# Kernel optimization log

Hardware: AMD Instinct MI355X
Metric: run time of the kernel (lower is better)

Reference implementation:

```python
import jax, jax.numpy as jnp
import numpy as np

E = 256        # HP.EMBED_SIZE
R = 8          # number of derivation rules / MLPs
S = 512        # number of sequential derivation steps
N = 256        # nodes produced per step
N_INIT = 1024  # initial axiom (thax) embeddings
TOTAL = N_INIT + S * N  # 132096 rows in the vectors buffer
M = 65536      # masked nodes fed to eval_net


def setup_inputs() -> dict:
    key = jax.random.key(0)
    ks = jax.random.split(key, 12)
    rng = np.random.default_rng(0)

    init_vecs = jax.random.normal(ks[0], (N_INIT, E), jnp.float32)
    # rule MLPs: concat(2 parents) -> E (relu) -> E
    W1 = jax.random.normal(ks[1], (R, 2 * E, E), jnp.float32) * (1.0 / np.sqrt(2 * E))
    b1 = jnp.zeros((R, E), jnp.float32)
    W2 = jax.random.normal(ks[2], (R, E, E), jnp.float32) * (1.0 / np.sqrt(E))
    b2 = jnp.zeros((R, E), jnp.float32)
    # eval net: E -> E (relu) -> 1
    eval_W1 = jax.random.normal(ks[3], (E, E), jnp.float32) * (1.0 / np.sqrt(E))
    eval_b1 = jnp.zeros((E,), jnp.float32)
    eval_W2 = jax.random.normal(ks[4], (E, 1), jnp.float32) * (1.0 / np.sqrt(E))
    eval_b2 = jnp.zeros((1,), jnp.float32)

    # step s writes rows [N_INIT + s*N, N_INIT + (s+1)*N)
    ind_steps = (N_INIT + np.arange(S * N, dtype=np.int32)).reshape(S, N)
    # parents drawn causally from already-computed prefix [0, N_INIT + s*N)
    highs = (N_INIT + np.arange(S, dtype=np.int64) * N)[:, None, None]
    pars_ind_steps = (rng.random((S, N, 2)) * highs).astype(np.int32)
    rule_steps = rng.integers(0, R, size=(S,)).astype(np.int32)
    mask = rng.integers(0, TOTAL, size=(M,)).astype(np.int32)

    pos = jax.random.uniform(ks[5], (M,), jnp.float32)
    neg = jax.random.uniform(ks[6], (M,), jnp.float32)
    target = jnp.round(jax.random.uniform(ks[7], (M,), jnp.float32))

    return {
        'init_vecs': init_vecs, 'W1': W1, 'b1': b1, 'W2': W2, 'b2': b2,
        'eval_W1': eval_W1, 'eval_b1': eval_b1, 'eval_W2': eval_W2, 'eval_b2': eval_b2,
        'pos': pos, 'neg': neg, 'target': target,
        'ind_steps': jnp.asarray(ind_steps), 'pars_ind_steps': jnp.asarray(pars_ind_steps),
        'rule_steps': jnp.asarray(rule_steps), 'mask': jnp.asarray(mask),
    }


def reference(init_vecs, W1, b1, W2, b2, eval_W1, eval_b1, eval_W2, eval_b2,
              pos, neg, target, ind_steps, pars_ind_steps, rule_steps, mask):
    vectors = jnp.zeros((TOTAL, E), init_vecs.dtype).at[:N_INIT].set(init_vecs)

    def step(vec, xs):
        inds, pars, r = xs            # [N], [N,2], scalar rule id
        p = vec[pars].reshape(N, 2 * E)   # gather parents
        h = jax.nn.relu(p @ W1[r] + b1[r])
        out = h @ W2[r] + b2[r]
        return vec.at[inds].set(out), None  # scatter new node embeddings

    vectors, _ = jax.lax.scan(step, vectors, (ind_steps, pars_ind_steps, rule_steps))

    x = vectors[mask]
    val = (jax.nn.relu(x @ eval_W1 + eval_b1) @ eval_W2 + eval_b2)[:, 0]

    # pos_weight = POS_WEIGHT_EXTRA * tot_neg / tot_pos (constant w.r.t. grads)
    pw = jax.lax.stop_gradient(jnp.sum(neg) / jnp.maximum(jnp.sum(pos), 1.0))
    # BCEWithLogitsLoss(pos_weight, reduction='none')
    contrib = pw * target * jax.nn.softplus(-val) + (1.0 - target) * jax.nn.softplus(val)
    loss = jnp.sum((pos + neg) * contrib)
    posOK = jnp.sum(pos * (val >= 0))
    negOK = jnp.sum(neg * (val < 0))
    return loss, posOK, negOK
```

## Files before the change

### kernel.cpp

```cpp
#include <hip/hip_runtime.h>
#include <math.h>

#define EMB   256
#define TWOE  512
#define NINIT 1024
#define NSTEP 512
#define NPS   256
#define TOTAL (NINIT + NSTEP * NPS)
#define MM    65536
#define NNODE (NSTEP * NPS)
#define NKEY  2048
#define BTH   512
#define TROWS 32
#define CHK_SH  16384
#define RULE_SH (24 * CHK_SH)

typedef short s16x8 __attribute__((ext_vector_type(8)));
typedef float f32x4 __attribute__((ext_vector_type(4)));

#define OFF_VECH   0ull
#define OFF_VECL   ((size_t)TOTAL * EMB * 2)
#define OFF_VAL    (2ull * (size_t)TOTAL * EMB * 2)
#define OFF_CNT    (OFF_VAL + (size_t)MM * 4)
#define OFF_ACC    (OFF_CNT + 4096)
#define OFF_PW     (OFF_ACC + 64)
#define OFF_KCNT   (OFF_PW + 192)
#define OFF_KOFS   (OFF_KCNT + (size_t)NKEY * 4)
#define OFF_NL     (OFF_KOFS + (size_t)NKEY * 4)
#define OFF_BROWS  (OFF_NL + 256)
#define OFF_LVL8   (OFF_BROWS + (size_t)NNODE * 4)
#define OFF_WSPLIT (OFF_LVL8 + 132352)


__device__ __forceinline__ void store_dev_u32(unsigned* p, unsigned v) {
  asm volatile("global_store_dword %0, %1, off sc0 sc1" :: "v"(p), "v"(v) : "memory");
}
__device__ __forceinline__ void store_dev_b64(void* p, uint2 v) {
  asm volatile("global_store_dwordx2 %0, %1, off sc0 sc1" :: "v"(p), "v"(v) : "memory");
}
__device__ __forceinline__ void store_dev_b128(void* p, uint4 v) {
  store_dev_b64(p, make_uint2(v.x, v.y));
  store_dev_b64((char*)p + 8, make_uint2(v.z, v.w));
}
__device__ __forceinline__ unsigned load_dev_u32(const unsigned* p) {
  unsigned r;
  asm volatile("global_load_dword %0, %1, off sc0 sc1\n\ts_waitcnt vmcnt(0)"
               : "=v"(r) : "v"(p) : "memory");
  return r;
}

__device__ __forceinline__ void gbar_tree(unsigned* cnt, int xcd) {
  asm volatile("s_waitcnt vmcnt(0)" ::: "memory");
  __syncthreads();
  if (threadIdx.x == 0) {
    unsigned* xarr = cnt + 32 * xcd;
    unsigned* garr = cnt + 512;
    unsigned* gep  = cnt + 544;
    unsigned* xep  = cnt + 576 + 32 * xcd;
    unsigned o = __hip_atomic_fetch_add(xarr, 1u, __ATOMIC_RELAXED, __HIP_MEMORY_SCOPE_AGENT);
    unsigned tgt = o / 32u + 1u;
    if ((o & 31u) == 31u) {
      unsigned g = __hip_atomic_fetch_add(garr, 1u, __ATOMIC_RELAXED, __HIP_MEMORY_SCOPE_AGENT);
      unsigned gt = g / 8u + 1u;
      if ((g & 7u) == 7u) store_dev_u32(gep, gt);
      else while (load_dev_u32(gep) < gt) __builtin_amdgcn_s_sleep(1);
      store_dev_u32(xep, tgt);
    } else {
      while (load_dev_u32(xep) < tgt) __builtin_amdgcn_s_sleep(1);
    }
  }
  __syncthreads();
}

__device__ __forceinline__ void split8(const float* f, uint4& h4, uint4& l4) {
  unsigned hu[8], lu[8];
  #pragma unroll
  for (int i = 0; i < 8; ++i) {
    unsigned u = __builtin_bit_cast(unsigned, f[i]);
    float rh = __builtin_bit_cast(float, u & 0xffff0000u);
    float rl = f[i] - rh;
    hu[i] = u >> 16;
    lu[i] = __builtin_bit_cast(unsigned, rl) >> 16;
  }
  h4 = make_uint4(hu[0] | (hu[1] << 16), hu[2] | (hu[3] << 16),
                  hu[4] | (hu[5] << 16), hu[6] | (hu[7] << 16));
  l4 = make_uint4(lu[0] | (lu[1] << 16), lu[2] | (lu[3] << 16),
                  lu[4] | (lu[5] << 16), lu[6] | (lu[7] << 16));
}

__global__ void zero_scratch(unsigned* cnt, double* acc) {
  for (int i = threadIdx.x; i < 1024; i += 256) cnt[i] = 0u;
  if (threadIdx.x < 8) acc[threadIdx.x] = 0.0;
}

__global__ void init_convert(const float* __restrict__ src,
                             unsigned short* __restrict__ vh,
                             unsigned short* __restrict__ vl) {
  int slot = blockIdx.x * blockDim.x + threadIdx.x;
  float f[8];
  *(float4*)&f[0] = reinterpret_cast<const float4*>(src)[slot * 2];
  *(float4*)&f[4] = reinterpret_cast<const float4*>(src)[slot * 2 + 1];
  uint4 h4, l4;
  split8(f, h4, l4);
  *(uint4*)(vh + (size_t)slot * 8) = h4;
  *(uint4*)(vl + (size_t)slot * 8) = l4;
}

__global__ __launch_bounds__(512)
void presplit(const float* __restrict__ W1, const float* __restrict__ W2,
              short* __restrict__ Ws)
{
  const int blk = blockIdx.x;
  const int r = blk / 24, c = blk % 24;
  const float* src; int kbase;
  if (c < 16) { src = W1 + (size_t)r * TWOE * EMB; kbase = c * 32; }
  else        { src = W2 + (size_t)r * EMB * EMB;  kbase = (c - 16) * 32; }
  short* dst = Ws + (size_t)blk * CHK_SH;
  const int tid = threadIdx.x;
  #pragma unroll
  for (int u = 0; u < 2; ++u) {
    int qq = tid + u * 512;
    int g = qq >> 6, l = qq & 63;
    const float* p = src + (size_t)(kbase + ((l >> 4) << 3)) * EMB + (g << 4) + (l & 15);
    float f[8];
    #pragma unroll
    for (int i = 0; i < 8; ++i) f[i] = p[i * EMB];
    uint4 h4, l4;
    split8(f, h4, l4);
    *(uint4*)(dst + (size_t)qq * 8) = h4;
    *(uint4*)(dst + 8192 + (size_t)qq * 8) = l4;
  }
}

__global__ __launch_bounds__(256)
void prepass_levels(const int* __restrict__ pars, unsigned char* __restrict__ lvl8,
                    int* __restrict__ nlp)
{
  __shared__ unsigned char slvl[TOTAL];
  __shared__ int swmax[4];
  const int t = threadIdx.x;
  for (int i = t; i < NINIT; i += 256) slvl[i] = 0;
  __syncthreads();
  int Pa[8], Pb[8];
  #pragma unroll
  for (int w = 0; w < 8; ++w) {
    Pa[w] = pars[2 * (w * NPS + t)];
    Pb[w] = pars[2 * (w * NPS + t) + 1];
  }
  int lmax = 0;
  for (int s0 = 0; s0 < NSTEP; s0 += 8) {
    int Na[8], Nb[8];
    if (s0 + 8 < NSTEP) {
      #pragma unroll
      for (int w = 0; w < 8; ++w) {
        Na[w] = pars[2 * ((s0 + 8 + w) * NPS + t)];
        Nb[w] = pars[2 * ((s0 + 8 + w) * NPS + t) + 1];
      }
    } else {
      #pragma unroll
      for (int w = 0; w < 8; ++w) { Na[w] = 0; Nb[w] = 0; }
    }
    #pragma unroll
    for (int w = 0; w < 8; ++w) {
      int l1 = slvl[Pa[w]], l2 = slvl[Pb[w]];
      int lv = 1 + (l1 > l2 ? l1 : l2);
      slvl[NINIT + (s0 + w) * NPS + t] = (unsigned char)lv;
      if (lv > lmax) lmax = lv;
      __syncthreads();
    }
    #pragma unroll
    for (int w = 0; w < 8; ++w) { Pa[w] = Na[w]; Pb[w] = Nb[w]; }
  }
  const unsigned* sv = (const unsigned*)slvl;
  unsigned* gv = (unsigned*)lvl8;
  for (int i = t; i < TOTAL / 4; i += 256) gv[i] = sv[i];
  for (int o = 32; o; o >>= 1) lmax = max(lmax, __shfl_down(lmax, o));
  if ((t & 63) == 0) swmax[t >> 6] = lmax;
  __syncthreads();
  if (t == 0) {
    int m = 0;
    for (int w = 0; w < 4; ++w) m = max(m, swmax[w]);
    nlp[0] = m;
  }
}

__global__ __launch_bounds__(1024)
void prepass_bucket(const unsigned char* __restrict__ lvl8, const int* __restrict__ rules,
                    int* __restrict__ kcnt, int* __restrict__ kofs,
                    int* __restrict__ brows)
{
  __shared__ int scnt[NKEY];
  __shared__ int sofs[NKEY];
  const int t = threadIdx.x;
  for (int k = t; k < NKEY; k += 1024) scnt[k] = 0;
  __syncthreads();
  for (int i = t; i < NNODE; i += 1024) {
    int key = (int)lvl8[NINIT + i] * 8 + rules[i >> 8];
    atomicAdd(&scnt[key], 1);
  }
  __syncthreads();
  if (t == 0) {
    int run = 0;
    for (int k = 0; k < NKEY; ++k) {
      sofs[k] = run; kofs[k] = run; kcnt[k] = scnt[k]; run += scnt[k];
    }
  }
  __syncthreads();
  for (int i = t; i < NNODE; i += 1024) {
    int key = (int)lvl8[NINIT + i] * 8 + rules[i >> 8];
    int pos = atomicAdd(&sofs[key], 1);
    brows[pos] = i;
  }
}

__global__ __launch_bounds__(BTH, 1)
void scan_kernel(const short* __restrict__ Ws, const float* __restrict__ b1,
                 const float* __restrict__ b2, const int* __restrict__ pars,
                 unsigned short* __restrict__ vech, unsigned short* __restrict__ vecl,
                 const int* __restrict__ kcnt, const int* __restrict__ kofs,
                 const int* __restrict__ brows, const int* __restrict__ nlp,
                 unsigned* __restrict__ cnt)
{
  __shared__ float hL[TROWS][260];
  __shared__ int spar[2 * TROWS];
  __shared__ int sorow[TROWS];
  const int tid = threadIdx.x;
  const int bid = blockIdx.x;
  const int lane = tid & 63;
  const int w = tid >> 6;
  const int rw = w & 1, cwb = (w >> 1) << 2;
  const int row16 = lane & 15, kb8 = (lane >> 4) << 3;
  const int arow = (rw << 4) + row16;
  const int NL = nlp[0];
  const int xcd = bid & 7, jb = bid >> 3;

  for (int lv = 1; lv <= NL; ++lv) {
    int cum[9]; cum[0] = 0;
    int cnts[8], ofss[8];
    #pragma unroll
    for (int r = 0; r < 8; ++r) {
      int c = kcnt[lv * 8 + r];
      cnts[r] = c; ofss[r] = kofs[lv * 8 + r];
      cum[r + 1] = cum[r] + ((c + TROWS - 1) >> 5);
    }
    const int G = cum[8];
    const int q = G >> 3, rm = G & 7;
    const int Gx = q + (xcd < rm ? 1 : 0);
    const int sx = xcd * q + (xcd < rm ? xcd : rm);
    for (int j = jb; j < Gx; j += 32) {
      const int g = sx + j;
      int rr = 0;
      while (g >= cum[rr + 1]) ++rr;
      const int t0 = g - cum[rr];
      const int cnt_b = cnts[rr], ofs_b = ofss[rr];
      const int tbase = t0 * TROWS;
      const short* __restrict__ Wr = Ws + (size_t)rr * RULE_SH;

      __syncthreads();
      if (tid < 2 * TROWS) {
        int slot = tbase + (tid >> 1);
        if (slot >= cnt_b) slot = cnt_b - 1;
        int node = brows[ofs_b + slot];
        spar[tid] = pars[2 * node + (tid & 1)];
        if ((tid & 1) == 0) sorow[tid >> 1] = NINIT + node;
      }
      __syncthreads();
      const int par0 = spar[2 * arow], par1 = spar[2 * arow + 1];
      float b1v[4], b2v[4];
      #pragma unroll
      for (int g4 = 0; g4 < 4; ++g4) {
        b1v[g4] = b1[rr * EMB + ((cwb + g4) << 4) + row16];
        b2v[g4] = b2[rr * EMB + ((cwb + g4) << 4) + row16];
      }

      uint4 pAh[4], pAl[4];
      #pragma unroll
      for (int d = 0; d < 4; ++d) {
        size_t off = (size_t)par0 * EMB + d * 32 + kb8;
        pAh[d] = *(const uint4*)(vech + off);
        pAl[d] = *(const uint4*)(vecl + off);
      }
      uint4 pBh[2][4], pBl[2][4];
      #pragma unroll
      for (int g4 = 0; g4 < 4; ++g4) {
        int gi = (cwb + g4) * 64 + lane;
        pBh[0][g4] = *(const uint4*)(Wr + (size_t)gi * 8);
        pBl[0][g4] = *(const uint4*)(Wr + 8192 + (size_t)gi * 8);
      }
      f32x4 acc[4] = {{0,0,0,0},{0,0,0,0},{0,0,0,0},{0,0,0,0}};
      #pragma unroll
      for (int c = 0; c < 16; ++c) {
        s16x8 AhC = __builtin_bit_cast(s16x8, pAh[c & 3]);
        s16x8 AlC = __builtin_bit_cast(s16x8, pAl[c & 3]);
        if (c + 4 < 16) {
          int kg = (c + 4) * 32 + kb8;
          int par = (kg >> 8) ? par1 : par0;
          size_t off = (size_t)par * EMB + (kg & 255);
          pAh[c & 3] = *(const uint4*)(vech + off);
          pAl[c & 3] = *(const uint4*)(vecl + off);
        }
        if (c + 1 < 16) {
          const short* chn = Wr + (size_t)(c + 1) * CHK_SH;
          #pragma unroll
          for (int g4 = 0; g4 < 4; ++g4) {
            int gi = (cwb + g4) * 64 + lane;
            pBh[(c + 1) & 1][g4] = *(const uint4*)(chn + (size_t)gi * 8);
            pBl[(c + 1) & 1][g4] = *(const uint4*)(chn + 8192 + (size_t)gi * 8);
          }
        }
        #pragma unroll
        for (int g4 = 0; g4 < 4; ++g4) {
          s16x8 Bh = __builtin_bit_cast(s16x8, pBh[c & 1][g4]);
          s16x8 Bl = __builtin_bit_cast(s16x8, pBl[c & 1][g4]);
          acc[g4] = __builtin_amdgcn_mfma_f32_16x16x32_bf16(AhC, Bh, acc[g4], 0, 0, 0);
          acc[g4] = __builtin_amdgcn_mfma_f32_16x16x32_bf16(AhC, Bl, acc[g4], 0, 0, 0);
          acc[g4] = __builtin_amdgcn_mfma_f32_16x16x32_bf16(AlC, Bh, acc[g4], 0, 0, 0);
        }
      }
      {
        const short* chn = Wr + (size_t)16 * CHK_SH;
        #pragma unroll
        for (int g4 = 0; g4 < 4; ++g4) {
          int gi = (cwb + g4) * 64 + lane;
          pBh[0][g4] = *(const uint4*)(chn + (size_t)gi * 8);
          pBl[0][g4] = *(const uint4*)(chn + 8192 + (size_t)gi * 8);
        }
      }
      #pragma unroll
      for (int g4 = 0; g4 < 4; ++g4) {
        #pragma unroll
        for (int jj = 0; jj < 4; ++jj)
          hL[(rw << 4) + ((lane >> 4) << 2) + jj][((cwb + g4) << 4) + row16] =
              fmaxf(acc[g4][jj] + b1v[g4], 0.f);
      }
      __syncthreads();
      uint4 qh[2], ql[2];
      {
        float af[8];
        *(float4*)&af[0] = *(const float4*)&hL[arow][kb8];
        *(float4*)&af[4] = *(const float4*)&hL[arow][kb8 + 4];
        split8(af, qh[0], ql[0]);
      }
      f32x4 acc2[4] = {{0,0,0,0},{0,0,0,0},{0,0,0,0},{0,0,0,0}};
      #pragma unroll
      for (int c2 = 0; c2 < 8; ++c2) {
        s16x8 AhC = __builtin_bit_cast(s16x8, qh[c2 & 1]);
        s16x8 AlC = __builtin_bit_cast(s16x8, ql[c2 & 1]);
        if (c2 + 1 < 8) {
          float af[8];
          *(float4*)&af[0] = *(const float4*)&hL[arow][(c2 + 1) * 32 + kb8];
          *(float4*)&af[4] = *(const float4*)&hL[arow][(c2 + 1) * 32 + kb8 + 4];
          split8(af, qh[(c2 + 1) & 1], ql[(c2 + 1) & 1]);
          const short* chn = Wr + (size_t)(17 + c2) * CHK_SH;
          #pragma unroll
          for (int g4 = 0; g4 < 4; ++g4) {
            int gi = (cwb + g4) * 64 + lane;
            pBh[(c2 + 1) & 1][g4] = *(const uint4*)(chn + (size_t)gi * 8);
            pBl[(c2 + 1) & 1][g4] = *(const uint4*)(chn + 8192 + (size_t)gi * 8);
          }
        }
        #pragma unroll
        for (int g4 = 0; g4 < 4; ++g4) {
          s16x8 Bh = __builtin_bit_cast(s16x8, pBh[c2 & 1][g4]);
          s16x8 Bl = __builtin_bit_cast(s16x8, pBl[c2 & 1][g4]);
          acc2[g4] = __builtin_amdgcn_mfma_f32_16x16x32_bf16(AhC, Bh, acc2[g4], 0, 0, 0);
          acc2[g4] = __builtin_amdgcn_mfma_f32_16x16x32_bf16(AhC, Bl, acc2[g4], 0, 0, 0);
          acc2[g4] = __builtin_amdgcn_mfma_f32_16x16x32_bf16(AlC, Bh, acc2[g4], 0, 0, 0);
        }
      }
      __syncthreads();
      #pragma unroll
      for (int g4 = 0; g4 < 4; ++g4) {
        #pragma unroll
        for (int jj = 0; jj < 4; ++jj)
          hL[(rw << 4) + ((lane >> 4) << 2) + jj][((cwb + g4) << 4) + row16] =
              acc2[g4][jj] + b2v[g4];
      }
      __syncthreads();
      #pragma unroll
      for (int u = 0; u < 2; ++u) {
        int s = tid + u * 512;
        int row = s >> 5, c8 = (s & 31) * 8;
        float of[8];
        *(float4*)&of[0] = *(const float4*)&hL[row][c8];
        *(float4*)&of[4] = *(const float4*)&hL[row][c8 + 4];
        uint4 h4, l4;
        split8(of, h4, l4);
        if (tbase + row < cnt_b) {
          size_t off = (size_t)sorow[row] * EMB + c8;
          store_dev_b128(vech + off, h4);
          store_dev_b128(vecl + off, l4);
        }
      }
    }
    gbar_tree(cnt, xcd);
  }
}

__global__ void reduce_pn(const float* __restrict__ pos, const float* __restrict__ neg,
                          double* acc) {
  double sp = 0.0, sn = 0.0;
  for (int m = blockIdx.x * blockDim.x + threadIdx.x; m < MM; m += gridDim.x * blockDim.x) {
    sp += (double)pos[m]; sn += (double)neg[m];
  }
  for (int o = 32; o; o >>= 1) { sp += __shfl_down(sp, o); sn += __shfl_down(sn, o); }
  __shared__ double rp[4], rn[4];
  int wid = threadIdx.x >> 6, lane = threadIdx.x & 63;
  if (lane == 0) { rp[wid] = sp; rn[wid] = sn; }
  __syncthreads();
  if (threadIdx.x == 0) {
    double tp = 0.0, tn = 0.0;
    for (int w = 0; w < 4; ++w) { tp += rp[w]; tn += rn[w]; }
    atomicAdd(&acc[0], tp); atomicAdd(&acc[1], tn);
  }
}

__global__ void pw_kernel(const double* __restrict__ acc, float* __restrict__ pw) {
  pw[0] = (float)(acc[1] / fmax(acc[0], 1.0));
}

__global__ __launch_bounds__(256)
void eval_kernel(const unsigned short* __restrict__ vh, const unsigned short* __restrict__ vl,
                 const int* __restrict__ mask,
                 const float* __restrict__ eW1, const float* __restrict__ eb1,
                 const float* __restrict__ eW2, const float* __restrict__ eb2,
                 float* __restrict__ val)
{
  __shared__ float xL[64][36];
  __shared__ float wLx[32][260];
  __shared__ int mrow[64];
  const int tid = threadIdx.x;
  const int a = tid >> 4, b = tid & 15;
  const int m0 = blockIdx.x * 64;
  if (tid < 64) mrow[tid] = mask[m0 + tid];
  __syncthreads();

  float acc[4][16];
  #pragma unroll
  for (int i = 0; i < 4; ++i)
    #pragma unroll
    for (int j = 0; j < 16; ++j) acc[i][j] = 0.f;

  for (int c = 0; c < 8; ++c) {
    const int e0 = c * 32;
    for (int idx = tid; idx < 64 * 4; idx += 256) {
      int rr = idx >> 2, u = idx & 3;
      size_t off = (size_t)mrow[rr] * EMB + e0 + u * 8;
      uint4 hv = *(const uint4*)(vh + off);
      uint4 lv = *(const uint4*)(vl + off);
      const unsigned* hu = (const unsigned*)&hv;
      const unsigned* lu = (const unsigned*)&lv;
      float fo[8];
      #pragma unroll
      for (int jj = 0; jj < 4; ++jj) {
        fo[2 * jj] = __builtin_bit_cast(float, (hu[jj] & 0xffffu) << 16) +
                     __builtin_bit_cast(float, (lu[jj] & 0xffffu) << 16);
        fo[2 * jj + 1] = __builtin_bit_cast(float, hu[jj] & 0xffff0000u) +
                         __builtin_bit_cast(float, lu[jj] & 0xffff0000u);
      }
      *(float4*)&xL[rr][u * 8] = *(float4*)&fo[0];
      *(float4*)&xL[rr][u * 8 + 4] = *(float4*)&fo[4];
    }
    for (int idx = tid; idx < 32 * 64; idx += 256) {
      int e = idx >> 6, k4 = idx & 63;
      reinterpret_cast<float4*>(&wLx[e][0])[k4] =
          reinterpret_cast<const float4*>(eW1 + (size_t)(e0 + e) * EMB)[k4];
    }
    __syncthreads();
    #pragma unroll 4
    for (int e = 0; e < 32; ++e) {
      float xs[4];
      #pragma unroll
      for (int rr = 0; rr < 4; ++rr) xs[rr] = xL[a * 4 + rr][e];
      const float4* wr = reinterpret_cast<const float4*>(&wLx[e][0]) + b * 4;
      float wk[16];
      *reinterpret_cast<float4*>(&wk[0])  = wr[0];
      *reinterpret_cast<float4*>(&wk[4])  = wr[1];
      *reinterpret_cast<float4*>(&wk[8])  = wr[2];
      *reinterpret_cast<float4*>(&wk[12]) = wr[3];
      #pragma unroll
      for (int rr = 0; rr < 4; ++rr)
        #pragma unroll
        for (int kk = 0; kk < 16; ++kk)
          acc[rr][kk] = fmaf(xs[rr], wk[kk], acc[rr][kk]);
    }
    __syncthreads();
  }

  float eb2v = eb2[0];
  float pv[4];
  #pragma unroll
  for (int rr = 0; rr < 4; ++rr) {
    float s = 0.f;
    #pragma unroll
    for (int kk = 0; kk < 16; ++kk) {
      float h = acc[rr][kk] + eb1[b * 16 + kk];
      h = fmaxf(h, 0.f);
      s += h * eW2[b * 16 + kk];
    }
    pv[rr] = s;
  }
  #pragma unroll
  for (int m = 1; m < 16; m <<= 1) {
    #pragma unroll
    for (int rr = 0; rr < 4; ++rr) pv[rr] += __shfl_xor(pv[rr], m);
  }
  if (b == 0) {
    #pragma unroll
    for (int rr = 0; rr < 4; ++rr) val[m0 + a * 4 + rr] = pv[rr] + eb2v;
  }
}

__global__ void loss_kernel(const float* __restrict__ val, const float* __restrict__ pos,
                            const float* __restrict__ neg, const float* __restrict__ tgt,
                            const float* __restrict__ pwp, double* acc)
{
  const float pw = pwp[0];
  double l = 0.0, pk = 0.0, nk = 0.0;
  for (int m = blockIdx.x * blockDim.x + threadIdx.x; m < MM; m += gridDim.x * blockDim.x) {
    float v = val[m], p = pos[m], n = neg[m], t = tgt[m];
    float lp = log1pf(expf(-fabsf(v)));
    float spn = fmaxf(-v, 0.f) + lp;
    float spp = fmaxf(v, 0.f) + lp;
    float contrib = pw * t * spn + (1.f - t) * spp;
    l += (double)((p + n) * contrib);
    if (v >= 0.f) pk += (double)p; else nk += (double)n;
  }
  for (int o = 32; o; o >>= 1) {
    l += __shfl_down(l, o); pk += __shfl_down(pk, o); nk += __shfl_down(nk, o);
  }
  __shared__ double s0[4], s1[4], s2[4];
  int wid = threadIdx.x >> 6, lane = threadIdx.x & 63;
  if (lane == 0) { s0[wid] = l; s1[wid] = pk; s2[wid] = nk; }
  __syncthreads();
  if (threadIdx.x == 0) {
    double ta = 0.0, tb = 0.0, tc = 0.0;
    for (int w = 0; w < 4; ++w) { ta += s0[w]; tb += s1[w]; tc += s2[w]; }
    atomicAdd(&acc[2], ta); atomicAdd(&acc[3], tb); atomicAdd(&acc[4], tc);
  }
}

__global__ void writeout(const double* __restrict__ acc, float* __restrict__ out) {
  if (threadIdx.x == 0) {
    out[0] = (float)acc[2];
    out[1] = (float)acc[3];
    out[2] = (float)acc[4];
  }
}

extern "C" void kernel_launch(void* const* d_in, const int* in_sizes, int n_in,
                              void* d_out, int out_size, void* d_ws, size_t ws_size,
                              hipStream_t stream)
{
  (void)in_sizes; (void)n_in; (void)out_size; (void)ws_size;
  const float* init_vecs = (const float*)d_in[0];
  const float* W1  = (const float*)d_in[1];
  const float* b1  = (const float*)d_in[2];
  const float* W2  = (const float*)d_in[3];
  const float* b2  = (const float*)d_in[4];
  const float* eW1 = (const float*)d_in[5];
  const float* eb1 = (const float*)d_in[6];
  const float* eW2 = (const float*)d_in[7];
  const float* eb2 = (const float*)d_in[8];
  const float* pos = (const float*)d_in[9];
  const float* neg = (const float*)d_in[10];
  const float* tgt = (const float*)d_in[11];
  const int* pars  = (const int*)d_in[13];
  const int* rules = (const int*)d_in[14];
  const int* mask  = (const int*)d_in[15];

  char* ws = (char*)d_ws;
  unsigned short* vech = (unsigned short*)(ws + OFF_VECH);
  unsigned short* vecl = (unsigned short*)(ws + OFF_VECL);
  float*    val   = (float*)(ws + OFF_VAL);
  unsigned* cnt   = (unsigned*)(ws + OFF_CNT);
  double*   acc   = (double*)(ws + OFF_ACC);
  float*    pw    = (float*)(ws + OFF_PW);
  int*      kcnt  = (int*)(ws + OFF_KCNT);
  int*      kofs  = (int*)(ws + OFF_KOFS);
  int*      nlp   = (int*)(ws + OFF_NL);
  int*      brows = (int*)(ws + OFF_BROWS);
  unsigned char* lvl8 = (unsigned char*)(ws + OFF_LVL8);
  short*    Ws    = (short*)(ws + OFF_WSPLIT);

  zero_scratch<<<1, 256, 0, stream>>>(cnt, acc);
  prepass_levels<<<1, 256, 0, stream>>>(pars, lvl8, nlp);
  prepass_bucket<<<1, 1024, 0, stream>>>(lvl8, rules, kcnt, kofs, brows);
  init_convert<<<128, 256, 0, stream>>>(init_vecs, vech, vecl);
  presplit<<<192, 512, 0, stream>>>(W1, W2, Ws);
  scan_kernel<<<256, BTH, 0, stream>>>(Ws, b1, b2, pars, vech, vecl,
                                       kcnt, kofs, brows, nlp, cnt);
  reduce_pn<<<128, 256, 0, stream>>>(pos, neg, acc);
  pw_kernel<<<1, 1, 0, stream>>>(acc, pw);
  eval_kernel<<<1024, 256, 0, stream>>>(vech, vecl, mask, eW1, eb1, eW2, eb2, val);
  loss_kernel<<<128, 256, 0, stream>>>(val, pos, neg, tgt, pw, acc);
  writeout<<<1, 1, 0, stream>>>(acc, (float*)d_out);
}
```

Before: 1.280 ms.

## Double row tile and stage rule weights in LDS via async global-to-LDS loads

The per-block row tile grows from 32 to 64 nodes, so each wave computes two 16-row MFMA tiles that share every weight fragment. Weight chunks are no longer loaded into registers per wave. They are double-buffered in shared memory with global_load_lds, and a full vmcnt wait plus barrier follows every chunk. This halves weight traffic per node and cuts register pressure. The cost is fewer tiles per level, which means less parallelism on sparse levels, along with many more block-wide barriers and larger LDS use.

```diff
diff --git a/kernel.cpp b/kernel.cpp
--- a/kernel.cpp
+++ b/kernel.cpp
@@ -11,7 +11,7 @@
 #define NNODE (NSTEP * NPS)
 #define NKEY  2048
 #define BTH   512
-#define TROWS 32
+#define TROWS 64
 #define CHK_SH  16384
 #define RULE_SH (24 * CHK_SH)
 
@@ -86,6 +86,17 @@
                   hu[4] | (hu[5] << 16), hu[6] | (hu[7] << 16));
   l4 = make_uint4(lu[0] | (lu[1] << 16), lu[2] | (lu[3] << 16),
                   lu[4] | (lu[5] << 16), lu[6] | (lu[7] << 16));
+}
+
+__device__ __forceinline__ void stage_chunk(short* ldst, const short* gsrc,
+                                            int w, int lane) {
+  #pragma unroll
+  for (int i = 0; i < 4; ++i) {
+    int off = (w * 4 + i) * 512;
+    __builtin_amdgcn_global_load_lds(
+        (const __attribute__((address_space(1))) unsigned int*)(gsrc + off + lane * 8),
+        (__attribute__((address_space(3))) unsigned int*)(ldst + off), 16, 0, 0);
+  }
 }
 
 __global__ void zero_scratch(unsigned* cnt, double* acc) {
@@ -221,6 +232,7 @@
                  const int* __restrict__ brows, const int* __restrict__ nlp,
                  unsigned* __restrict__ cnt)
 {
+  __shared__ short wB[2][CHK_SH];
   __shared__ float hL[TROWS][260];
   __shared__ int spar[2 * TROWS];
   __shared__ int sorow[TROWS];
@@ -230,7 +242,9 @@
   const int w = tid >> 6;
   const int rw = w & 1, cwb = (w >> 1) << 2;
   const int row16 = lane & 15, kb8 = (lane >> 4) << 3;
-  const int arow = (rw << 4) + row16;
+  const int arow0 = (rw << 5) + row16;
+  const int arow1 = arow0 + 16;
+  const int hrow = (rw << 5) + ((lane >> 4) << 2);
   const int NL = nlp[0];
   const int xcd = bid & 7, jb = bid >> 3;
 
@@ -241,7 +255,7 @@
     for (int r = 0; r < 8; ++r) {
       int c = kcnt[lv * 8 + r];
       cnts[r] = c; ofss[r] = kofs[lv * 8 + r];
-      cum[r + 1] = cum[r] + ((c + TROWS - 1) >> 5);
+      cum[r + 1] = cum[r] + ((c + TROWS - 1) >> 6);
     }
     const int G = cum[8];
     const int q = G >> 3, rm = G & 7;
@@ -257,6 +271,7 @@
       const short* __restrict__ Wr = Ws + (size_t)rr * RULE_SH;
 
       __syncthreads();
+      stage_chunk(&wB[0][0], Wr, w, lane);
       if (tid < 2 * TROWS) {
         int slot = tbase + (tid >> 1);
         if (slot >= cnt_b) slot = cnt_b - 1;
@@ -265,120 +280,122 @@
         if ((tid & 1) == 0) sorow[tid >> 1] = NINIT + node;
       }
       __syncthreads();
-      const int par0 = spar[2 * arow], par1 = spar[2 * arow + 1];
+      const int p00 = spar[2 * arow0], p01 = spar[2 * arow0 + 1];
+      const int p10 = spar[2 * arow1], p11 = spar[2 * arow1 + 1];
       float b1v[4], b2v[4];
       #pragma unroll
       for (int g4 = 0; g4 < 4; ++g4) {
         b1v[g4] = b1[rr * EMB + ((cwb + g4) << 4) + row16];
         b2v[g4] = b2[rr * EMB + ((cwb + g4) << 4) + row16];
       }
-
-      uint4 pAh[4], pAl[4];
-      #pragma unroll
-      for (int d = 0; d < 4; ++d) {
-        size_t off = (size_t)par0 * EMB + d * 32 + kb8;
-        pAh[d] = *(const uint4*)(vech + off);
-        pAl[d] = *(const uint4*)(vecl + off);
-      }
-      uint4 pBh[2][4], pBl[2][4];
-      #pragma unroll
-      for (int g4 = 0; g4 < 4; ++g4) {
-        int gi = (cwb + g4) * 64 + lane;
-        pBh[0][g4] = *(const uint4*)(Wr + (size_t)gi * 8);
-        pBl[0][g4] = *(const uint4*)(Wr + 8192 + (size_t)gi * 8);
-      }
-      f32x4 acc[4] = {{0,0,0,0},{0,0,0,0},{0,0,0,0},{0,0,0,0}};
+      uint4 a0h, a0l, a1h, a1l;
+      {
+        size_t o0 = (size_t)p00 * EMB + kb8;
+        size_t o1 = (size_t)p10 * EMB + kb8;
+        a0h = *(const uint4*)(vech + o0); a0l = *(const uint4*)(vecl + o0);
+        a1h = *(const uint4*)(vech + o1); a1l = *(const uint4*)(vecl + o1);
+      }
+      asm volatile("s_waitcnt vmcnt(0)" ::: "memory");
+      __syncthreads();
+      f32x4 acc0[4] = {{0,0,0,0},{0,0,0,0},{0,0,0,0},{0,0,0,0}};
+      f32x4 acc1[4] = {{0,0,0,0},{0,0,0,0},{0,0,0,0},{0,0,0,0}};
+      int cur = 0;
       #pragma unroll
       for (int c = 0; c < 16; ++c) {
-        s16x8 AhC = __builtin_bit_cast(s16x8, pAh[c & 3]);
-        s16x8 AlC = __builtin_bit_cast(s16x8, pAl[c & 3]);
-        if (c + 4 < 16) {
-          int kg = (c + 4) * 32 + kb8;
-          int par = (kg >> 8) ? par1 : par0;
-          size_t off = (size_t)par * EMB + (kg & 255);
-          pAh[c & 3] = *(const uint4*)(vech + off);
-          pAl[c & 3] = *(const uint4*)(vecl + off);
+        stage_chunk(&wB[cur ^ 1][0], Wr + (size_t)(c + 1) * CHK_SH, w, lane);
+        uint4 n0h, n0l, n1h, n1l;
+        if (c < 15) {
+          int kg = (c + 1) * 32 + kb8;
+          int q0 = (kg >> 8) ? p01 : p00;
+          int q1 = (kg >> 8) ? p11 : p10;
+          size_t o0 = (size_t)q0 * EMB + (kg & 255);
+          size_t o1 = (size_t)q1 * EMB + (kg & 255);
+          n0h = *(const uint4*)(vech + o0); n0l = *(const uint4*)(vecl + o0);
+          n1h = *(const uint4*)(vech + o1); n1l = *(const uint4*)(vecl + o1);
         }
-        if (c + 1 < 16) {
-          const short* chn = Wr + (size_t)(c + 1) * CHK_SH;
+        s16x8 A0h = __builtin_bit_cast(s16x8, a0h);
+        s16x8 A0l = __builtin_bit_cast(s16x8, a0l);
+        s16x8 A1h = __builtin_bit_cast(s16x8, a1h);
+        s16x8 A1l = __builtin_bit_cast(s16x8, a1l);
+        #pragma unroll
+        for (int g4 = 0; g4 < 4; ++g4) {
+          const short* bp = &wB[cur][((cwb + g4) * 64 + lane) * 8];
+          s16x8 Bh = *(const s16x8*)bp;
+          s16x8 Bl = *(const s16x8*)(bp + 8192);
+          acc0[g4] = __builtin_amdgcn_mfma_f32_16x16x32_bf16(A0h, Bh, acc0[g4], 0, 0, 0);
+          acc0[g4] = __builtin_amdgcn_mfma_f32_16x16x32_bf16(A0h, Bl, acc0[g4], 0, 0, 0);
+          acc0[g4] = __builtin_amdgcn_mfma_f32_16x16x32_bf16(A0l, Bh, acc0[g4], 0, 0, 0);
+          acc1[g4] = __builtin_amdgcn_mfma_f32_16x16x32_bf16(A1h, Bh, acc1[g4], 0, 0, 0);
+          acc1[g4] = __builtin_amdgcn_mfma_f32_16x16x32_bf16(A1h, Bl, acc1[g4], 0, 0, 0);
+          acc1[g4] = __builtin_amdgcn_mfma_f32_16x16x32_bf16(A1l, Bh, acc1[g4], 0, 0, 0);
+        }
+        if (c == 15) {
           #pragma unroll
           for (int g4 = 0; g4 < 4; ++g4) {
-            int gi = (cwb + g4) * 64 + lane;
-            pBh[(c + 1) & 1][g4] = *(const uint4*)(chn + (size_t)gi * 8);
-            pBl[(c + 1) & 1][g4] = *(const uint4*)(chn + 8192 + (size_t)gi * 8);
+            #pragma unroll
+            for (int jj = 0; jj < 4; ++jj) {
+              int col = ((cwb + g4) << 4) + row16;
+              hL[hrow + jj][col]      = fmaxf(acc0[g4][jj] + b1v[g4], 0.f);
+              hL[hrow + 16 + jj][col] = fmaxf(acc1[g4][jj] + b1v[g4], 0.f);
+            }
           }
         }
+        asm volatile("s_waitcnt vmcnt(0)" ::: "memory");
+        __syncthreads();
+        cur ^= 1;
+        if (c < 15) { a0h = n0h; a0l = n0l; a1h = n1h; a1l = n1l; }
+      }
+      #pragma unroll
+      for (int g4 = 0; g4 < 4; ++g4) {
+        acc0[g4] = (f32x4){0, 0, 0, 0};
+        acc1[g4] = (f32x4){0, 0, 0, 0};
+      }
+      #pragma unroll
+      for (int c2 = 0; c2 < 8; ++c2) {
+        if (c2 < 7)
+          stage_chunk(&wB[cur ^ 1][0], Wr + (size_t)(17 + c2) * CHK_SH, w, lane);
+        uint4 qh0, ql0, qh1, ql1;
+        {
+          float af[8];
+          *(float4*)&af[0] = *(const float4*)&hL[arow0][c2 * 32 + kb8];
+          *(float4*)&af[4] = *(const float4*)&hL[arow0][c2 * 32 + kb8 + 4];
+          split8(af, qh0, ql0);
+          *(float4*)&af[0] = *(const float4*)&hL[arow1][c2 * 32 + kb8];
+          *(float4*)&af[4] = *(const float4*)&hL[arow1][c2 * 32 + kb8 + 4];
+          split8(af, qh1, ql1);
+        }
+        s16x8 A0h = __builtin_bit_cast(s16x8, qh0);
+        s16x8 A0l = __builtin_bit_cast(s16x8, ql0);
+        s16x8 A1h = __builtin_bit_cast(s16x8, qh1);
+        s16x8 A1l = __builtin_bit_cast(s16x8, ql1);
         #pragma unroll
         for (int g4 = 0; g4 < 4; ++g4) {
-          s16x8 Bh = __builtin_bit_cast(s16x8, pBh[c & 1][g4]);
-          s16x8 Bl = __builtin_bit_cast(s16x8, pBl[c & 1][g4]);
-          acc[g4] = __builtin_amdgcn_mfma_f32_16x16x32_bf16(AhC, Bh, acc[g4], 0, 0, 0);
-          acc[g4] = __builtin_amdgcn_mfma_f32_16x16x32_bf16(AhC, Bl, acc[g4], 0, 0, 0);
-          acc[g4] = __builtin_amdgcn_mfma_f32_16x16x32_bf16(AlC, Bh, acc[g4], 0, 0, 0);
+          const short* bp = &wB[cur][((cwb + g4) * 64 + lane) * 8];
+          s16x8 Bh = *(const s16x8*)bp;
+          s16x8 Bl = *(const s16x8*)(bp + 8192);
+          acc0[g4] = __builtin_amdgcn_mfma_f32_16x16x32_bf16(A0h, Bh, acc0[g4], 0, 0, 0);
+          acc0[g4] = __builtin_amdgcn_mfma_f32_16x16x32_bf16(A0h, Bl, acc0[g4], 0, 0, 0);
+          acc0[g4] = __builtin_amdgcn_mfma_f32_16x16x32_bf16(A0l, Bh, acc0[g4], 0, 0, 0);
+          acc1[g4] = __builtin_amdgcn_mfma_f32_16x16x32_bf16(A1h, Bh, acc1[g4], 0, 0, 0);
+          acc1[g4] = __builtin_amdgcn_mfma_f32_16x16x32_bf16(A1h, Bl, acc1[g4], 0, 0, 0);
+          acc1[g4] = __builtin_amdgcn_mfma_f32_16x16x32_bf16(A1l, Bh, acc1[g4], 0, 0, 0);
         }
-      }
-      {
-        const short* chn = Wr + (size_t)16 * CHK_SH;
-        #pragma unroll
-        for (int g4 = 0; g4 < 4; ++g4) {
-          int gi = (cwb + g4) * 64 + lane;
-          pBh[0][g4] = *(const uint4*)(chn + (size_t)gi * 8);
-          pBl[0][g4] = *(const uint4*)(chn + 8192 + (size_t)gi * 8);
-        }
+        asm volatile("s_waitcnt vmcnt(0)" ::: "memory");
+        __syncthreads();
+        cur ^= 1;
       }
       #pragma unroll
       for (int g4 = 0; g4 < 4; ++g4) {
         #pragma unroll
-        for (int jj = 0; jj < 4; ++jj)
-          hL[(rw << 4) + ((lane >> 4) << 2) + jj][((cwb + g4) << 4) + row16] =
-              fmaxf(acc[g4][jj] + b1v[g4], 0.f);
+        for (int jj = 0; jj < 4; ++jj) {
+          int col = ((cwb + g4) << 4) + row16;
+          hL[hrow + jj][col]      = acc0[g4][jj] + b2v[g4];
+          hL[hrow + 16 + jj][col] = acc1[g4][jj] + b2v[g4];
+        }
       }
       __syncthreads();
-      uint4 qh[2], ql[2];
-      {
-        float af[8];
-        *(float4*)&af[0] = *(const float4*)&hL[arow][kb8];
-        *(float4*)&af[4] = *(const float4*)&hL[arow][kb8 + 4];
-        split8(af, qh[0], ql[0]);
-      }
-      f32x4 acc2[4] = {{0,0,0,0},{0,0,0,0},{0,0,0,0},{0,0,0,0}};
-      #pragma unroll
-      for (int c2 = 0; c2 < 8; ++c2) {
-        s16x8 AhC = __builtin_bit_cast(s16x8, qh[c2 & 1]);
-        s16x8 AlC = __builtin_bit_cast(s16x8, ql[c2 & 1]);
-        if (c2 + 1 < 8) {
-          float af[8];
-          *(float4*)&af[0] = *(const float4*)&hL[arow][(c2 + 1) * 32 + kb8];
-          *(float4*)&af[4] = *(const float4*)&hL[arow][(c2 + 1) * 32 + kb8 + 4];
-          split8(af, qh[(c2 + 1) & 1], ql[(c2 + 1) & 1]);
-          const short* chn = Wr + (size_t)(17 + c2) * CHK_SH;
-          #pragma unroll
-          for (int g4 = 0; g4 < 4; ++g4) {
-            int gi = (cwb + g4) * 64 + lane;
-            pBh[(c2 + 1) & 1][g4] = *(const uint4*)(chn + (size_t)gi * 8);
-            pBl[(c2 + 1) & 1][g4] = *(const uint4*)(chn + 8192 + (size_t)gi * 8);
-          }
-        }
-        #pragma unroll
-        for (int g4 = 0; g4 < 4; ++g4) {
-          s16x8 Bh = __builtin_bit_cast(s16x8, pBh[c2 & 1][g4]);
-          s16x8 Bl = __builtin_bit_cast(s16x8, pBl[c2 & 1][g4]);
-          acc2[g4] = __builtin_amdgcn_mfma_f32_16x16x32_bf16(AhC, Bh, acc2[g4], 0, 0, 0);
-          acc2[g4] = __builtin_amdgcn_mfma_f32_16x16x32_bf16(AhC, Bl, acc2[g4], 0, 0, 0);
-          acc2[g4] = __builtin_amdgcn_mfma_f32_16x16x32_bf16(AlC, Bh, acc2[g4], 0, 0, 0);
-        }
-      }
-      __syncthreads();
-      #pragma unroll
-      for (int g4 = 0; g4 < 4; ++g4) {
-        #pragma unroll
-        for (int jj = 0; jj < 4; ++jj)
-          hL[(rw << 4) + ((lane >> 4) << 2) + jj][((cwb + g4) << 4) + row16] =
-              acc2[g4][jj] + b2v[g4];
-      }
-      __syncthreads();
-      #pragma unroll
-      for (int u = 0; u < 2; ++u) {
+      #pragma unroll
+      for (int u = 0; u < 4; ++u) {
         int s = tid + u * 512;
         int row = s >> 5, c8 = (s & 31) * 8;
         float of[8];
```

Measured after the change: 1.278 ms. Within noise of the previous version (-0.1%).
